# Kernel optimization log

Measured on AMD Instinct MI355X. Metric: run time of the kernel, lower is better.

## Reference

```python
import jax, jax.numpy as jnp
import numpy as np

B, S, H, HD = 2, 4096, 8, 64
D = H * HD
EPS = 1e-5

def setup_inputs() -> dict:
    key = jax.random.key(0)
    ks = jax.random.split(key, 8)
    sc = 0.05
    return {
        "x": jax.random.normal(ks[0], (B, S, D), jnp.float32),
        "y": jax.random.normal(ks[1], (B, S, D), jnp.float32),
        "Wk": jax.random.normal(ks[2], (H, HD, HD), jnp.float32) * sc,
        "bk": jax.random.normal(ks[3], (H, HD), jnp.float32) * sc,
        "Wq": jax.random.normal(ks[4], (H, HD, HD), jnp.float32) * sc,
        "bq": jax.random.normal(ks[5], (H, HD), jnp.float32) * sc,
        "Wv": jax.random.normal(ks[6], (H, HD, HD), jnp.float32) * sc,
        "bv": jax.random.normal(ks[7], (H, HD), jnp.float32) * sc,
        "gamma": jnp.ones((D,), jnp.float32),
        "beta": jnp.zeros((D,), jnp.float32),
    }

def reference(x, y, Wk, bk, Wq, bq, Wv, bv, gamma, beta):
    b, s, d = x.shape
    # slice-per-head == reshape to [B,S,H,HD]
    xh = x.reshape(b, s, H, HD)
    yh = y.reshape(b, s, H, HD)
    # per-head linear projections (batched over heads)
    K = jnp.einsum('bshd,hde->bshe', xh, Wk) + bk  # [B,S,H,HD]
    Q = jnp.einsum('bshd,hde->bshe', yh, Wq) + bq
    V = jnp.einsum('bshd,hde->bshe', xh, Wv) + bv
    scale = 1.0 / jnp.sqrt(jnp.float32(HD))
    scores = jnp.einsum('bshe,bthe->bhst', Q, K) * scale  # [B,H,S,S]
    attn = jax.nn.softmax(scores, axis=-1)
    out = jnp.einsum('bhst,bthe->bshe', attn, V)  # [B,S,H,HD]
    out = out.reshape(b, s, d) + y
    # LayerNorm over last dim
    mu = jnp.mean(out, axis=-1, keepdims=True)
    var = jnp.mean(jnp.square(out - mu), axis=-1, keepdims=True)
    return (out - mu) * jax.lax.rsqrt(var + EPS) * gamma + beta
```

## Files before the change

### kernel.cpp

```cpp
#include <hip/hip_runtime.h>
#include <hip/hip_bf16.h>

#define B_  2
#define S_  4096
#define H_  8
#define HD_ 64
#define D_  512
#define NSPLIT 2
#define NT_ ((S_ / NSPLIT) / 64)

using bf16x8 = __attribute__((ext_vector_type(8))) short;
using f32x4  = __attribute__((ext_vector_type(4))) float;
using f32x16 = __attribute__((ext_vector_type(16))) float;
using u32x4  = __attribute__((ext_vector_type(4))) unsigned int;

__device__ __forceinline__ unsigned short f2bf(float f) {
    unsigned int u = __float_as_uint(f);
    u += 0x7FFFu + ((u >> 16) & 1u);
    return (unsigned short)(u >> 16);
}

__device__ __forceinline__ float bf2f(short s) {
    return __uint_as_float(((unsigned int)(unsigned short)s) << 16);
}

__device__ __forceinline__ unsigned int pkbf(float a, float b) {
    unsigned int r;
    asm("v_cvt_pk_bf16_f32 %0, %1, %2" : "=v"(r) : "v"(a), "v"(b));
    return r;
}

__device__ __forceinline__ float ex2(float x) {
    float r;
    asm("v_exp_f32 %0, %1" : "=v"(r) : "v"(x));
    return r;
}

__device__ __forceinline__ void gl16(const unsigned short* g, unsigned short* l) {
    __builtin_amdgcn_global_load_lds(
        (const __attribute__((address_space(1))) unsigned int*)g,
        (__attribute__((address_space(3))) unsigned int*)l, 16, 0, 0);
}

__global__ __launch_bounds__(256) void proj_kernel(
    const float* __restrict__ x,  const float* __restrict__ yy,
    const float* __restrict__ Wk, const float* __restrict__ bk,
    const float* __restrict__ Wq, const float* __restrict__ bq,
    const float* __restrict__ Wv, const float* __restrict__ bv,
    unsigned short* __restrict__ Qw, unsigned short* __restrict__ Kw,
    unsigned short* __restrict__ Vt)
{
    __shared__ __attribute__((aligned(16))) unsigned short xs[64][72];
    __shared__ __attribute__((aligned(16))) unsigned short ys[64][72];
    __shared__ __attribute__((aligned(16))) unsigned short wtk[64][72];
    __shared__ __attribute__((aligned(16))) unsigned short wtq[64][72];
    __shared__ __attribute__((aligned(16))) unsigned short wtv[64][72];
    __shared__ __attribute__((aligned(16))) unsigned short vtl[64][72];

    const int t  = threadIdx.x;
    const int s0 = blockIdx.x * 64;
    const int bh = blockIdx.y;
    const int b  = bh >> 3, h = bh & 7;

    #pragma unroll
    for (int i = 0; i < 4; ++i) {
        int id = t + 256 * i;
        int row = id >> 4, c4 = id & 15;
        size_t ga = ((size_t)(b * S_ + s0 + row)) * D_ + h * HD_ + c4 * 4;
        float4 xv = *(const float4*)(x + ga);
        float4 yv = *(const float4*)(yy + ga);
        unsigned int xl = f2bf(xv.x) | ((unsigned int)f2bf(xv.y) << 16);
        unsigned int xh = f2bf(xv.z) | ((unsigned int)f2bf(xv.w) << 16);
        unsigned int yl = f2bf(yv.x) | ((unsigned int)f2bf(yv.y) << 16);
        unsigned int yh = f2bf(yv.z) | ((unsigned int)f2bf(yv.w) << 16);
        *(uint2*)&xs[row][c4 * 4] = make_uint2(xl, xh);
        *(uint2*)&ys[row][c4 * 4] = make_uint2(yl, yh);
    }
    #pragma unroll
    for (int i = 0; i < 4; ++i) {
        int id = t + 256 * i;
        int dd = id >> 4, e4 = id & 15;
        size_t wa = (size_t)(h * HD_ + dd) * HD_ + e4 * 4;
        float4 wk4 = *(const float4*)(Wk + wa);
        float4 wq4 = *(const float4*)(Wq + wa);
        float4 wv4 = *(const float4*)(Wv + wa);
        wtk[e4*4+0][dd] = f2bf(wk4.x); wtk[e4*4+1][dd] = f2bf(wk4.y);
        wtk[e4*4+2][dd] = f2bf(wk4.z); wtk[e4*4+3][dd] = f2bf(wk4.w);
        wtq[e4*4+0][dd] = f2bf(wq4.x); wtq[e4*4+1][dd] = f2bf(wq4.y);
        wtq[e4*4+2][dd] = f2bf(wq4.z); wtq[e4*4+3][dd] = f2bf(wq4.w);
        wtv[e4*4+0][dd] = f2bf(wv4.x); wtv[e4*4+1][dd] = f2bf(wv4.y);
        wtv[e4*4+2][dd] = f2bf(wv4.z); wtv[e4*4+3][dd] = f2bf(wv4.w);
    }
    __syncthreads();

    const int lane = t & 63, w = t >> 6;
    const int g = lane >> 4, lq = lane & 15;

    bf16x8 ax[2], ay[2];
    #pragma unroll
    for (int kk = 0; kk < 2; ++kk) {
        ax[kk] = *(const bf16x8*)&xs[w*16 + lq][kk*32 + g*8];
        ay[kk] = *(const bf16x8*)&ys[w*16 + lq][kk*32 + g*8];
    }
    __syncthreads();

    f32x4 ak[4], aq[4], av[4];
    #pragma unroll
    for (int n = 0; n < 4; ++n) { ak[n] = (f32x4)0.f; aq[n] = (f32x4)0.f; av[n] = (f32x4)0.f; }

    #pragma unroll
    for (int n = 0; n < 4; ++n) {
        #pragma unroll
        for (int kk = 0; kk < 2; ++kk) {
            bf16x8 bk_ = *(const bf16x8*)&wtk[n*16 + lq][kk*32 + g*8];
            ak[n] = __builtin_amdgcn_mfma_f32_16x16x32_bf16(ax[kk], bk_, ak[n], 0, 0, 0);
            bf16x8 bq_ = *(const bf16x8*)&wtq[n*16 + lq][kk*32 + g*8];
            aq[n] = __builtin_amdgcn_mfma_f32_16x16x32_bf16(ay[kk], bq_, aq[n], 0, 0, 0);
            bf16x8 bv_ = *(const bf16x8*)&wtv[n*16 + lq][kk*32 + g*8];
            av[n] = __builtin_amdgcn_mfma_f32_16x16x32_bf16(ax[kk], bv_, av[n], 0, 0, 0);
        }
    }

    const float cscale = 0.125f * 1.44269504088896340736f;
    #pragma unroll
    for (int n = 0; n < 4; ++n) {
        int e = n*16 + lq;
        float bkv = bk[h*HD_ + e], bqv = bq[h*HD_ + e], bvv = bv[h*HD_ + e];
        #pragma unroll
        for (int r = 0; r < 4; ++r) {
            int srow = w*16 + g*4 + r;
            xs[srow][e]  = f2bf(ak[n][r] + bkv);
            ys[srow][e]  = f2bf((aq[n][r] + bqv) * cscale);
            vtl[e][srow] = f2bf(av[n][r] + bvv);
        }
    }
    __syncthreads();
    #pragma unroll
    for (int i = 0; i < 2; ++i) {
        int id = t + 256 * i;
        int rr = id >> 3, c = id & 7;
        bf16x8 kv = *(const bf16x8*)&xs[rr][c*8];
        *(bf16x8*)(Kw + ((size_t)bh * S_ + s0 + rr) * HD_ + c*8) = kv;
        bf16x8 qv = *(const bf16x8*)&ys[rr][c*8];
        *(bf16x8*)(Qw + ((size_t)bh * S_ + s0 + rr) * HD_ + c*8) = qv;
        bf16x8 vv = *(const bf16x8*)&vtl[rr][c*8];
        *(bf16x8*)(Vt + ((size_t)bh * HD_ + rr) * S_ + s0 + c*8) = vv;
    }
}

__global__ __launch_bounds__(256, 2) void attn_kernel(
    const unsigned short* __restrict__ Qw, const unsigned short* __restrict__ Kw,
    const unsigned short* __restrict__ Vt, unsigned short* __restrict__ U,
    float* __restrict__ sbuf)
{
    __shared__ __attribute__((aligned(16))) unsigned short smem[4][64][64];

    const int t = threadIdx.x, lane = t & 63, w = t >> 6;
    const int lx = lane & 31, hi = lane >> 5;
    const int q0 = blockIdx.x * 256;
    const int bh = blockIdx.y;
    const int z  = blockIdx.z;
    const int b  = bh >> 3, h = bh & 7;
    const int kvbase = z * (S_ / NSPLIT);

    const unsigned short* Kb = Kw + ((size_t)bh * S_ + kvbase) * HD_;
    const unsigned short* Vb = Vt + (size_t)bh * HD_ * S_ + kvbase;

    bf16x8 qfA[4], qfB[4];
    #pragma unroll
    for (int kq = 0; kq < 4; ++kq) {
        qfA[kq] = *(const bf16x8*)(Qw + ((size_t)bh*S_ + q0 + w*64 + lx)*HD_ + kq*16 + hi*8);
        qfB[kq] = *(const bf16x8*)(Qw + ((size_t)bh*S_ + q0 + w*64 + 32 + lx)*HD_ + kq*16 + hi*8);
    }

    f32x16 oA0 = (f32x16)0.f, oA1 = (f32x16)0.f;
    f32x16 oB0 = (f32x16)0.f, oB1 = (f32x16)0.f;
    float ssA = 0.f, ssB = 0.f;

    const int w16 = w * 16;
    const int sw8 = ((lane & 7) ^ (lane >> 3)) * 8;
    const unsigned short* kg0 = Kb + (size_t)(w16 +     (lane >> 3)) * HD_ + sw8;
    const unsigned short* kg1 = Kb + (size_t)(w16 + 8 + (lane >> 3)) * HD_ + sw8;
    const unsigned short* vg0 = Vb + (size_t)(w16 +     (lane >> 3)) * S_  + sw8;
    const unsigned short* vg1 = Vb + (size_t)(w16 + 8 + (lane >> 3)) * S_  + sw8;

    gl16(kg0, &smem[0][w16][0]);     gl16(kg1, &smem[0][w16 + 8][0]);
    gl16(vg0, &smem[2][w16][0]);     gl16(vg1, &smem[2][w16 + 8][0]);
    kg0 += 64 * HD_; kg1 += 64 * HD_; vg0 += 64; vg1 += 64;
    __syncthreads();

#define TILE(CUR, KT)                                                         \
    {                                                                         \
        if ((KT) + 1 < NT_) {                                                 \
            gl16(kg0, &smem[(CUR)^1][w16][0]);                                \
            gl16(kg1, &smem[(CUR)^1][w16 + 8][0]);                            \
            gl16(vg0, &smem[2+((CUR)^1)][w16][0]);                            \
            gl16(vg1, &smem[2+((CUR)^1)][w16 + 8][0]);                        \
            kg0 += 64 * HD_; kg1 += 64 * HD_; vg0 += 64; vg1 += 64;           \
        }                                                                     \
        __builtin_amdgcn_s_setprio(1);                                        \
        f32x16 sA0 = (f32x16)0.f, sA1 = (f32x16)0.f;                          \
        f32x16 sB0 = (f32x16)0.f, sB1 = (f32x16)0.f;                          \
        _Pragma("unroll")                                                     \
        for (int kq = 0; kq < 4; ++kq) {                                      \
            bf16x8 kf0 = *(const bf16x8*)&smem[CUR][lx][(kq*16 + hi*8) ^ ((lx & 7)*8)]; \
            sA0 = __builtin_amdgcn_mfma_f32_32x32x16_bf16(kf0, qfA[kq], sA0, 0, 0, 0); \
            sB0 = __builtin_amdgcn_mfma_f32_32x32x16_bf16(kf0, qfB[kq], sB0, 0, 0, 0); \
            bf16x8 kf1 = *(const bf16x8*)&smem[CUR][32 + lx][(kq*16 + hi*8) ^ ((lx & 7)*8)]; \
            sA1 = __builtin_amdgcn_mfma_f32_32x32x16_bf16(kf1, qfA[kq], sA1, 0, 0, 0); \
            sB1 = __builtin_amdgcn_mfma_f32_32x32x16_bf16(kf1, qfB[kq], sB1, 0, 0, 0); \
        }                                                                     \
        float tA = 0.f, tB = 0.f;                                             \
        _Pragma("unroll")                                                     \
        for (int r = 0; r < 16; ++r) {                                        \
            sA0[r] = ex2(sA0[r]); sA1[r] = ex2(sA1[r]);                       \
            sB0[r] = ex2(sB0[r]); sB1[r] = ex2(sB1[r]);                       \
            tA += sA0[r] + sA1[r]; tB += sB0[r] + sB1[r];                     \
        }                                                                     \
        ssA += tA; ssB += tB;                                                 \
        _Pragma("unroll")                                                     \
        for (int ks = 0; ks < 4; ++ks) {                                      \
            const int u0 = (ks & 1) * 2;                                      \
            unsigned int a0, a1, a2, a3, b0, b1, b2, b3;                      \
            if (ks < 2) {                                                     \
                a0 = pkbf(sA0[4*u0+0],     sA0[4*u0+1]);                      \
                a2 = pkbf(sA0[4*(u0+1)+0], sA0[4*(u0+1)+1]);                  \
                a1 = pkbf(sA0[4*u0+2],     sA0[4*u0+3]);                      \
                a3 = pkbf(sA0[4*(u0+1)+2], sA0[4*(u0+1)+3]);                  \
                b0 = pkbf(sB0[4*u0+0],     sB0[4*u0+1]);                      \
                b2 = pkbf(sB0[4*(u0+1)+0], sB0[4*(u0+1)+1]);                  \
                b1 = pkbf(sB0[4*u0+2],     sB0[4*u0+3]);                      \
                b3 = pkbf(sB0[4*(u0+1)+2], sB0[4*(u0+1)+3]);                  \
            } else {                                                          \
                a0 = pkbf(sA1[4*u0+0],     sA1[4*u0+1]);                      \
                a2 = pkbf(sA1[4*(u0+1)+0], sA1[4*(u0+1)+1]);                  \
                a1 = pkbf(sA1[4*u0+2],     sA1[4*u0+3]);                      \
                a3 = pkbf(sA1[4*(u0+1)+2], sA1[4*(u0+1)+3]);                  \
                b0 = pkbf(sB1[4*u0+0],     sB1[4*u0+1]);                      \
                b2 = pkbf(sB1[4*(u0+1)+0], sB1[4*(u0+1)+1]);                  \
                b1 = pkbf(sB1[4*u0+2],     sB1[4*u0+3]);                      \
                b3 = pkbf(sB1[4*(u0+1)+2], sB1[4*(u0+1)+3]);                  \
            }                                                                 \
            asm("v_permlane32_swap_b32 %0, %1" : "+v"(a0), "+v"(a2));         \
            asm("v_permlane32_swap_b32 %0, %1" : "+v"(a1), "+v"(a3));         \
            asm("v_permlane32_swap_b32 %0, %1" : "+v"(b0), "+v"(b2));         \
            asm("v_permlane32_swap_b32 %0, %1" : "+v"(b1), "+v"(b3));         \
            u32x4 pwA; pwA.x = a0; pwA.y = a1; pwA.z = a2; pwA.w = a3;        \
            u32x4 pwB; pwB.x = b0; pwB.y = b1; pwB.z = b2; pwB.w = b3;        \
            bf16x8 pA = __builtin_bit_cast(bf16x8, pwA);                      \
            bf16x8 pB = __builtin_bit_cast(bf16x8, pwB);                      \
            bf16x8 vf0 = *(const bf16x8*)&smem[2+(CUR)][lx][(ks*16 + hi*8) ^ ((lx & 7)*8)]; \
            bf16x8 vf1 = *(const bf16x8*)&smem[2+(CUR)][32 + lx][(ks*16 + hi*8) ^ (((32+lx) & 7)*8)]; \
            oA0 = __builtin_amdgcn_mfma_f32_32x32x16_bf16(vf0, pA, oA0, 0, 0, 0); \
            oB0 = __builtin_amdgcn_mfma_f32_32x32x16_bf16(vf0, pB, oB0, 0, 0, 0); \
            oA1 = __builtin_amdgcn_mfma_f32_32x32x16_bf16(vf1, pA, oA1, 0, 0, 0); \
            oB1 = __builtin_amdgcn_mfma_f32_32x32x16_bf16(vf1, pB, oB1, 0, 0, 0); \
        }                                                                     \
        __builtin_amdgcn_s_setprio(0);                                        \
        __syncthreads();                                                      \
    }

    for (int kt = 0; kt < NT_; kt += 2) {
        TILE(0, kt)
        TILE(1, kt + 1)
    }
#undef TILE

    ssA += __shfl_xor(ssA, 32);
    ssB += __shfl_xor(ssB, 32);
    unsigned short* osh = &smem[0][0][0] + w * 4096;
    const int rloc = lane >> 3;
    const int dcol = (lane & 7) * 8;

#define OUT_GROUP(OG0, OG1, SS, G32)                                          \
    {                                                                         \
        _Pragma("unroll")                                                     \
        for (int d0 = 0; d0 < 2; ++d0)                                        \
            _Pragma("unroll")                                                 \
            for (int u = 0; u < 4; ++u) {                                     \
                unsigned int lo = pkbf((d0 ? OG1 : OG0)[4*u+0], (d0 ? OG1 : OG0)[4*u+1]); \
                unsigned int hw = pkbf((d0 ? OG1 : OG0)[4*u+2], (d0 ? OG1 : OG0)[4*u+3]); \
                int d = d0*32 + 8*u + 4*hi;                                   \
                *(uint2*)&osh[lx*64 + (d ^ ((lx & 7)*8))] = make_uint2(lo, hw); \
            }                                                                 \
        unsigned short* ubase = U + (size_t)z * (B_*S_*(size_t)D_)            \
                                  + ((size_t)b * S_ + q0 + w*64 + (G32)) * D_ + h * HD_; \
        _Pragma("unroll")                                                     \
        for (int i = 0; i < 4; ++i) {                                         \
            int q = i*8 + rloc;                                               \
            bf16x8 ov = *(const bf16x8*)&osh[q*64 + (dcol ^ ((q & 7)*8))];    \
            *(bf16x8*)(ubase + (size_t)q * D_ + dcol) = ov;                   \
        }                                                                     \
        if (hi == 0) {                                                        \
            const int qrow = q0 + w*64 + (G32) + lx;                          \
            sbuf[(size_t)z * (B_*S_*H_) + ((size_t)b * S_ + qrow) * H_ + h] = (SS); \
        }                                                                     \
    }

    OUT_GROUP(oA0, oA1, ssA, 0)
    OUT_GROUP(oB0, oB1, ssB, 32)
#undef OUT_GROUP
}

__global__ __launch_bounds__(256) void ln_kernel(
    const unsigned short* __restrict__ U, const float* __restrict__ sbuf,
    const float* __restrict__ yy,
    const float* __restrict__ gamma, const float* __restrict__ beta,
    float* __restrict__ out)
{
    const int t = threadIdx.x, lane = t & 63, w = t >> 6;
    const size_t row = (size_t)blockIdx.x * 4 + w;
    const int h = lane >> 3;

    float s0 = sbuf[row * H_ + h];
    float s1 = sbuf[(size_t)(B_*S_)*H_ + row * H_ + h];
    float inv = 1.0f / (s0 + s1);

    bf16x8 u0 = *(const bf16x8*)(U + row * D_ + lane*8);
    bf16x8 u1 = *(const bf16x8*)(U + (size_t)(B_*S_)*(size_t)D_ + row * D_ + lane*8);
    const float* yr = yy + row * D_;

    float v[8];
    #pragma unroll
    for (int i = 0; i < 2; ++i) {
        float4 yv = *(const float4*)(yr + lane*8 + i*4);
        v[i*4+0] = (bf2f(u0[i*4+0]) + bf2f(u1[i*4+0]))*inv + yv.x;
        v[i*4+1] = (bf2f(u0[i*4+1]) + bf2f(u1[i*4+1]))*inv + yv.y;
        v[i*4+2] = (bf2f(u0[i*4+2]) + bf2f(u1[i*4+2]))*inv + yv.z;
        v[i*4+3] = (bf2f(u0[i*4+3]) + bf2f(u1[i*4+3]))*inv + yv.w;
    }
    float s = 0.f;
    #pragma unroll
    for (int j = 0; j < 8; ++j) s += v[j];
    #pragma unroll
    for (int o = 32; o >= 1; o >>= 1) s += __shfl_xor(s, o);
    float mu = s * (1.f / 512.f);
    float qs = 0.f;
    #pragma unroll
    for (int j = 0; j < 8; ++j) { float d = v[j] - mu; qs += d * d; }
    #pragma unroll
    for (int o = 32; o >= 1; o >>= 1) qs += __shfl_xor(qs, o);
    float rstd = rsqrtf(qs * (1.f / 512.f) + 1e-5f);

    #pragma unroll
    for (int i = 0; i < 2; ++i) {
        float4 gm = *(const float4*)(gamma + lane*8 + i*4);
        float4 bt = *(const float4*)(beta  + lane*8 + i*4);
        float4 o4;
        o4.x = (v[i*4+0] - mu) * rstd * gm.x + bt.x;
        o4.y = (v[i*4+1] - mu) * rstd * gm.y + bt.y;
        o4.z = (v[i*4+2] - mu) * rstd * gm.z + bt.z;
        o4.w = (v[i*4+3] - mu) * rstd * gm.w + bt.w;
        *(float4*)(out + row * D_ + lane*8 + i*4) = o4;
    }
}

extern "C" void kernel_launch(void* const* d_in, const int* in_sizes, int n_in,
                              void* d_out, int out_size, void* d_ws, size_t ws_size,
                              hipStream_t stream) {
    const float* x     = (const float*)d_in[0];
    const float* y     = (const float*)d_in[1];
    const float* Wk    = (const float*)d_in[2];
    const float* bk    = (const float*)d_in[3];
    const float* Wq    = (const float*)d_in[4];
    const float* bq    = (const float*)d_in[5];
    const float* Wv    = (const float*)d_in[6];
    const float* bv    = (const float*)d_in[7];
    const float* gamma = (const float*)d_in[8];
    const float* beta  = (const float*)d_in[9];

    const size_t NTOK = (size_t)B_ * H_ * S_ * HD_;
    unsigned short* Qw = (unsigned short*)d_ws;
    unsigned short* Kw = Qw + NTOK;
    unsigned short* Vt = Kw + NTOK;
    unsigned short* U  = Vt + NTOK;
    float* sbuf = (float*)(U + (size_t)NSPLIT * B_ * S_ * D_);

    dim3 pgrid(S_ / 64, B_ * H_);
    proj_kernel<<<pgrid, 256, 0, stream>>>(x, y, Wk, bk, Wq, bq, Wv, bv, Qw, Kw, Vt);
    dim3 agrid(S_ / 256, B_ * H_, NSPLIT);
    attn_kernel<<<agrid, 256, 0, stream>>>(Qw, Kw, Vt, U, sbuf);
    ln_kernel<<<(B_ * S_) / 4, 256, 0, stream>>>(U, sbuf, y, gamma, beta, (float*)d_out);
}
```

Measured before the change: 96.91 us.

## Triple-buffer K/V tiles with vmcnt-based waits and prefetch distance two

Replaces the double-buffered K/V LDS pipeline with a three-stage ring, so global-to-LDS loads run two tiles ahead. Each tile now waits with an explicit s_waitcnt vmcnt and a raw s_barrier instead of a trailing __syncthreads. The goal is to hide more global load latency behind the MFMA work. In exchange LDS use rises from 32KB to 48KB per block, which may limit occupancy under launch_bounds(256,2), and the hardcoded 32-tile loop schedule ties correctness to NT_.

```diff
diff --git a/kernel.cpp b/kernel.cpp
--- a/kernel.cpp
+++ b/kernel.cpp
@@ -153,7 +153,7 @@
     const unsigned short* __restrict__ Vt, unsigned short* __restrict__ U,
     float* __restrict__ sbuf)
 {
-    __shared__ __attribute__((aligned(16))) unsigned short smem[4][64][64];
+    __shared__ __attribute__((aligned(16))) unsigned short smem[6][64][64];
 
     const int t = threadIdx.x, lane = t & 63, w = t >> 6;
     const int lx = lane & 31, hi = lane >> 5;
@@ -184,29 +184,31 @@
     const unsigned short* vg0 = Vb + (size_t)(w16 +     (lane >> 3)) * S_  + sw8;
     const unsigned short* vg1 = Vb + (size_t)(w16 + 8 + (lane >> 3)) * S_  + sw8;
 
-    gl16(kg0, &smem[0][w16][0]);     gl16(kg1, &smem[0][w16 + 8][0]);
-    gl16(vg0, &smem[2][w16][0]);     gl16(vg1, &smem[2][w16 + 8][0]);
-    kg0 += 64 * HD_; kg1 += 64 * HD_; vg0 += 64; vg1 += 64;
-    __syncthreads();
-
-#define TILE(CUR, KT)                                                         \
+#define STAGE(BUF)                                                            \
     {                                                                         \
-        if ((KT) + 1 < NT_) {                                                 \
-            gl16(kg0, &smem[(CUR)^1][w16][0]);                                \
-            gl16(kg1, &smem[(CUR)^1][w16 + 8][0]);                            \
-            gl16(vg0, &smem[2+((CUR)^1)][w16][0]);                            \
-            gl16(vg1, &smem[2+((CUR)^1)][w16 + 8][0]);                        \
-            kg0 += 64 * HD_; kg1 += 64 * HD_; vg0 += 64; vg1 += 64;           \
-        }                                                                     \
+        gl16(kg0, &smem[BUF][w16][0]);     gl16(kg1, &smem[BUF][w16 + 8][0]); \
+        gl16(vg0, &smem[3+(BUF)][w16][0]); gl16(vg1, &smem[3+(BUF)][w16 + 8][0]); \
+        kg0 += 64 * HD_; kg1 += 64 * HD_; vg0 += 64; vg1 += 64;               \
+    }
+
+    STAGE(0)
+    STAGE(1)
+
+#define TILE(BUF, SB, VMN)                                                    \
+    {                                                                         \
+        asm volatile("s_waitcnt vmcnt(" #VMN ")" ::: "memory");               \
+        __builtin_amdgcn_sched_barrier(0);                                    \
+        __builtin_amdgcn_s_barrier();                                         \
+        if ((SB) >= 0) STAGE(SB)                                              \
         __builtin_amdgcn_s_setprio(1);                                        \
         f32x16 sA0 = (f32x16)0.f, sA1 = (f32x16)0.f;                          \
         f32x16 sB0 = (f32x16)0.f, sB1 = (f32x16)0.f;                          \
         _Pragma("unroll")                                                     \
         for (int kq = 0; kq < 4; ++kq) {                                      \
-            bf16x8 kf0 = *(const bf16x8*)&smem[CUR][lx][(kq*16 + hi*8) ^ ((lx & 7)*8)]; \
+            bf16x8 kf0 = *(const bf16x8*)&smem[BUF][lx][(kq*16 + hi*8) ^ ((lx & 7)*8)]; \
             sA0 = __builtin_amdgcn_mfma_f32_32x32x16_bf16(kf0, qfA[kq], sA0, 0, 0, 0); \
             sB0 = __builtin_amdgcn_mfma_f32_32x32x16_bf16(kf0, qfB[kq], sB0, 0, 0, 0); \
-            bf16x8 kf1 = *(const bf16x8*)&smem[CUR][32 + lx][(kq*16 + hi*8) ^ ((lx & 7)*8)]; \
+            bf16x8 kf1 = *(const bf16x8*)&smem[BUF][32 + lx][(kq*16 + hi*8) ^ ((lx & 7)*8)]; \
             sA1 = __builtin_amdgcn_mfma_f32_32x32x16_bf16(kf1, qfA[kq], sA1, 0, 0, 0); \
             sB1 = __builtin_amdgcn_mfma_f32_32x32x16_bf16(kf1, qfB[kq], sB1, 0, 0, 0); \
         }                                                                     \
@@ -249,22 +251,27 @@
             u32x4 pwB; pwB.x = b0; pwB.y = b1; pwB.z = b2; pwB.w = b3;        \
             bf16x8 pA = __builtin_bit_cast(bf16x8, pwA);                      \
             bf16x8 pB = __builtin_bit_cast(bf16x8, pwB);                      \
-            bf16x8 vf0 = *(const bf16x8*)&smem[2+(CUR)][lx][(ks*16 + hi*8) ^ ((lx & 7)*8)]; \
-            bf16x8 vf1 = *(const bf16x8*)&smem[2+(CUR)][32 + lx][(ks*16 + hi*8) ^ (((32+lx) & 7)*8)]; \
+            bf16x8 vf0 = *(const bf16x8*)&smem[3+(BUF)][lx][(ks*16 + hi*8) ^ ((lx & 7)*8)]; \
+            bf16x8 vf1 = *(const bf16x8*)&smem[3+(BUF)][32 + lx][(ks*16 + hi*8) ^ (((32+lx) & 7)*8)]; \
             oA0 = __builtin_amdgcn_mfma_f32_32x32x16_bf16(vf0, pA, oA0, 0, 0, 0); \
             oB0 = __builtin_amdgcn_mfma_f32_32x32x16_bf16(vf0, pB, oB0, 0, 0, 0); \
             oA1 = __builtin_amdgcn_mfma_f32_32x32x16_bf16(vf1, pA, oA1, 0, 0, 0); \
             oB1 = __builtin_amdgcn_mfma_f32_32x32x16_bf16(vf1, pB, oB1, 0, 0, 0); \
         }                                                                     \
         __builtin_amdgcn_s_setprio(0);                                        \
-        __syncthreads();                                                      \
-    }
-
-    for (int kt = 0; kt < NT_; kt += 2) {
-        TILE(0, kt)
-        TILE(1, kt + 1)
-    }
+    }
+
+    for (int it = 0; it < 10; ++it) {
+        TILE(0, 2, 4)
+        TILE(1, 0, 4)
+        TILE(2, 1, 4)
+    }
+    TILE(0, -1, 4)
+    TILE(1, -1, 0)
 #undef TILE
+#undef STAGE
+
+    __syncthreads();
 
     ssA += __shfl_xor(ssA, 32);
     ssB += __shfl_xor(ssB, 32);
```

New measurement: 122.4 us. 1.26x slower.
